# Kernel tuning notes

Hardware: AMD Instinct MI355X
Metric: run time of the kernel (lower is better)

## Reference

```python
import jax, jax.numpy as jnp
import numpy as np

EMBED = 1024
HEADS = 16
HEAD_DIM = EMBED // HEADS


def setup_inputs() -> dict:
    key = jax.random.key(0)
    k1, k2, k3 = jax.random.split(key, 3)
    return {
        "hidden_states": jax.random.normal(k1, (2, 2048, EMBED), dtype=jnp.float32),
        "c_attn_w": jax.random.normal(k2, (EMBED, 3 * EMBED), dtype=jnp.float32) * 0.02,
        "c_attn_b": jnp.zeros((3 * EMBED,), dtype=jnp.float32),
        "c_proj_w": jax.random.normal(k3, (EMBED, EMBED), dtype=jnp.float32) * 0.02,
        "c_proj_b": jnp.zeros((EMBED,), dtype=jnp.float32),
    }


def reference(hidden_states, c_attn_w, c_attn_b, c_proj_w, c_proj_b):
    B, S, E = hidden_states.shape
    H, D = HEADS, HEAD_DIM
    qkv = hidden_states @ c_attn_w + c_attn_b  # [B,S,3E]
    q, k, v = jnp.split(qkv, 3, axis=-1)
    # split heads -> [B,H,S,D]
    def split_heads(t):
        return t.reshape(B, S, H, D).transpose(0, 2, 1, 3)
    q, k, v = split_heads(q), split_heads(k), split_heads(v)
    scores = jnp.einsum("bhqd,bhkd->bhqk", q, k) / jnp.asarray(D ** 0.5, q.dtype)
    causal = jnp.tril(jnp.ones((S, S), dtype=bool))[None, None]
    mask_value = jnp.finfo(scores.dtype).min
    scores = jnp.where(causal, scores, mask_value)
    attn_weights = jax.nn.softmax(scores, axis=-1)  # [B,H,S,S]
    attn_out = jnp.einsum("bhqk,bhkd->bhqd", attn_weights, v)
    attn_out = attn_out.transpose(0, 2, 1, 3).reshape(B, S, E)
    attn_out = attn_out @ c_proj_w + c_proj_b
    return attn_out, attn_weights
```

## Files before the change

### kernel.cpp

```cpp
#include <hip/hip_runtime.h>
#include <hip/hip_bf16.h>

#define EMBED 1024
#define HEADS 16
#define HEAD_DIM 64
#define BATCH 2
#define SEQ 2048
#define MROWS (BATCH*SEQ)
#define NQKV  (3*EMBED)

typedef __attribute__((ext_vector_type(8))) short short8;
typedef __attribute__((ext_vector_type(4))) float float4v;

static __device__ __forceinline__ short f2bf(float f) {
    union { float f; unsigned u; } x; x.f = f;
    unsigned r = (x.u + 0x7FFFu + ((x.u >> 16) & 1u)) >> 16;
    return (short)r;
}

__global__ __launch_bounds__(256) void cast_bf16_k(const float* __restrict__ in,
                                                   short* __restrict__ out, int n8) {
    int i = blockIdx.x * 256 + threadIdx.x;
    if (i >= n8) return;
    const float4* p = (const float4*)in + (size_t)i * 2;
    float4 a = p[0], b = p[1];
    short8 o;
    o[0] = f2bf(a.x); o[1] = f2bf(a.y); o[2] = f2bf(a.z); o[3] = f2bf(a.w);
    o[4] = f2bf(b.x); o[5] = f2bf(b.y); o[6] = f2bf(b.z); o[7] = f2bf(b.w);
    *((short8*)out + i) = o;
}

__global__ __launch_bounds__(256) void transpose_cast_k(const float* __restrict__ W,
                                                        short* __restrict__ Wt,
                                                        int K, int N) {
    __shared__ float tile[32][33];
    int tx = threadIdx.x & 31, ty = threadIdx.x >> 5;
    int n0 = blockIdx.x * 32, k0 = blockIdx.y * 32;
#pragma unroll
    for (int i = 0; i < 4; i++)
        tile[ty + i * 8][tx] = W[(size_t)(k0 + ty + i * 8) * N + n0 + tx];
    __syncthreads();
#pragma unroll
    for (int i = 0; i < 4; i++)
        Wt[(size_t)(n0 + ty + i * 8) * K + k0 + tx] = f2bf(tile[tx][ty + i * 8]);
}

__global__ __launch_bounds__(256) void gemm_bf16_k(const short* __restrict__ A,
                                                   const short* __restrict__ Bt,
                                                   const float* __restrict__ bias,
                                                   float* __restrict__ outF,
                                                   short* __restrict__ outB,
                                                   int M, int N, int K) {
    __shared__ __align__(16) short As[64 * 40];
    __shared__ __align__(16) short Bs[64 * 40];
    const int tid = threadIdx.x;
    const int wave = tid >> 6, lane = tid & 63, quad = lane >> 4, l16 = lane & 15;
    const int m0 = blockIdx.x * 64, n0 = blockIdx.y * 64;

    float4v acc[4];
#pragma unroll
    for (int i = 0; i < 4; i++) acc[i] = (float4v){0.f, 0.f, 0.f, 0.f};

    const int r = tid >> 2, c8 = (tid & 3) * 8;
    for (int k0 = 0; k0 < K; k0 += 32) {
        __syncthreads();
        *(short8*)&As[r * 40 + c8] = *(const short8*)&A[(size_t)(m0 + r) * K + k0 + c8];
        *(short8*)&Bs[r * 40 + c8] = *(const short8*)&Bt[(size_t)(n0 + r) * K + k0 + c8];
        __syncthreads();
        short8 a = *(const short8*)&As[(wave * 16 + l16) * 40 + quad * 8];
#pragma unroll
        for (int ns = 0; ns < 4; ns++) {
            short8 b = *(const short8*)&Bs[(ns * 16 + l16) * 40 + quad * 8];
            acc[ns] = __builtin_amdgcn_mfma_f32_16x16x32_bf16(a, b, acc[ns], 0, 0, 0);
        }
    }
#pragma unroll
    for (int ns = 0; ns < 4; ns++) {
        int col = n0 + ns * 16 + l16;
        float bv = bias ? bias[col] : 0.f;
#pragma unroll
        for (int i = 0; i < 4; i++) {
            int row = m0 + wave * 16 + quad * 4 + i;
            float v = acc[ns][i] + bv;
            if (outF) outF[(size_t)row * N + col] = v;
            else      outB[(size_t)row * N + col] = f2bf(v);
        }
    }
}

__global__ __launch_bounds__(256) void attn_k(const short* __restrict__ qkv,
                                              float* __restrict__ wout,
                                              short* __restrict__ aheads) {
    __shared__ __align__(16) short Qs[32 * 72];
    __shared__ __align__(16) short Ks[32 * 72];
    __shared__ __align__(16) short Vt[64 * 40];
    __shared__ __align__(16) short Ps[32 * 40];
    __shared__ float Mred[2][32], Lred[2][32], Mfin[32], Lfin[32];

    const int tid = threadIdx.x;
    const int wave = tid >> 6, lane = tid & 63, quad = lane >> 4, l16 = lane & 15;
    const int qs = wave >> 1, ks = wave & 1;
    const int bh = blockIdx.x & 31;
    const int b = bh >> 4, h = bh & 15;
    const int qt = 63 - (blockIdx.x >> 5);
    const int q0 = qt * 32;
    const int kend = q0 + 32;
    const int nch = kend >> 5;

    const short* qbase = qkv + (size_t)(b * SEQ) * NQKV + h * 64;
    const short* kbase = qbase + EMBED;
    const short* vbase = qbase + 2 * EMBED;
    float* wrow = wout + ((size_t)bh * SEQ + q0) * SEQ;

    {
        int r = tid >> 3, c8 = (tid & 7) * 8;
        *(short8*)&Qs[r * 72 + c8] = *(const short8*)&qbase[(size_t)(q0 + r) * NQKV + c8];
    }
    __syncthreads();
    const short8 aq0 = *(const short8*)&Qs[(qs * 16 + l16) * 72 + quad * 8];
    const short8 aq1 = *(const short8*)&Qs[(qs * 16 + l16) * 72 + 32 + quad * 8];

    const int kcol = ks * 16 + l16;
    float mrun[4], lrun[4];
#pragma unroll
    for (int i = 0; i < 4; i++) { mrun[i] = -1e30f; lrun[i] = 0.f; }

    for (int c = 0; c < nch; c++) {
        int kc = c * 32;
        __syncthreads();
        {
            int r = tid >> 3, c8 = (tid & 7) * 8;
            *(short8*)&Ks[r * 72 + c8] = *(const short8*)&kbase[(size_t)(kc + r) * NQKV + c8];
        }
        __syncthreads();
        short8 bk0 = *(const short8*)&Ks[(ks * 16 + l16) * 72 + quad * 8];
        short8 bk1 = *(const short8*)&Ks[(ks * 16 + l16) * 72 + 32 + quad * 8];
        float4v acc = (float4v){0.f, 0.f, 0.f, 0.f};
        acc = __builtin_amdgcn_mfma_f32_16x16x32_bf16(aq0, bk0, acc, 0, 0, 0);
        acc = __builtin_amdgcn_mfma_f32_16x16x32_bf16(aq1, bk1, acc, 0, 0, 0);
        int kg = kc + kcol;
#pragma unroll
        for (int i = 0; i < 4; i++) {
            int qg = q0 + qs * 16 + quad * 4 + i;
            if (kg <= qg) {
                float s = acc[i] * 0.125f;
                float mn = fmaxf(mrun[i], s);
                lrun[i] = lrun[i] * __expf(mrun[i] - mn) + __expf(s - mn);
                mrun[i] = mn;
            }
        }
    }
#pragma unroll
    for (int i = 0; i < 4; i++) {
        float m = mrun[i], l = lrun[i];
#pragma unroll
        for (int off = 1; off <= 8; off <<= 1) {
            float mo = __shfl_xor(m, off);
            float lo = __shfl_xor(l, off);
            float mn = fmaxf(m, mo);
            l = l * __expf(m - mn) + lo * __expf(mo - mn);
            m = mn;
        }
        mrun[i] = m; lrun[i] = l;
    }
    if (l16 == 0) {
#pragma unroll
        for (int i = 0; i < 4; i++) {
            Mred[ks][qs * 16 + quad * 4 + i] = mrun[i];
            Lred[ks][qs * 16 + quad * 4 + i] = lrun[i];
        }
    }
    __syncthreads();
    if (tid < 32) {
        float m0 = Mred[0][tid], m1 = Mred[1][tid];
        float mn = fmaxf(m0, m1);
        float L = Lred[0][tid] * __expf(m0 - mn) + Lred[1][tid] * __expf(m1 - mn);
        Mfin[tid] = mn;
        Lfin[tid] = 1.0f / L;
    }
    __syncthreads();
    float Mi[4], Li[4];
#pragma unroll
    for (int i = 0; i < 4; i++) {
        Mi[i] = Mfin[qs * 16 + quad * 4 + i];
        Li[i] = Lfin[qs * 16 + quad * 4 + i];
    }

    float4v oacc0 = (float4v){0.f, 0.f, 0.f, 0.f};
    float4v oacc1 = (float4v){0.f, 0.f, 0.f, 0.f};
    const int dhalf = ks;
    for (int c = 0; c < nch; c++) {
        int kc = c * 32;
        __syncthreads();
        {
            int r = tid >> 3, c8 = (tid & 7) * 8;
            *(short8*)&Ks[r * 72 + c8] = *(const short8*)&kbase[(size_t)(kc + r) * NQKV + c8];
            int vk = tid & 31, dg = tid >> 5;
            short8 v8 = *(const short8*)&vbase[(size_t)(kc + vk) * NQKV + dg * 8];
#pragma unroll
            for (int i = 0; i < 8; i++) Vt[(dg * 8 + i) * 40 + vk] = v8[i];
        }
        __syncthreads();
        short8 bk0 = *(const short8*)&Ks[(ks * 16 + l16) * 72 + quad * 8];
        short8 bk1 = *(const short8*)&Ks[(ks * 16 + l16) * 72 + 32 + quad * 8];
        float4v acc = (float4v){0.f, 0.f, 0.f, 0.f};
        acc = __builtin_amdgcn_mfma_f32_16x16x32_bf16(aq0, bk0, acc, 0, 0, 0);
        acc = __builtin_amdgcn_mfma_f32_16x16x32_bf16(aq1, bk1, acc, 0, 0, 0);
        int kg = kc + kcol;
#pragma unroll
        for (int i = 0; i < 4; i++) {
            int lrow = qs * 16 + quad * 4 + i;
            int qg = q0 + lrow;
            float p = 0.f;
            if (kg <= qg) p = __expf(acc[i] * 0.125f - Mi[i]) * Li[i];
            wrow[(size_t)lrow * SEQ + kg] = p;
            Ps[lrow * 40 + ks * 16 + l16] = f2bf(p);
        }
        __syncthreads();
        short8 ap  = *(const short8*)&Ps[(qs * 16 + l16) * 40 + quad * 8];
        short8 bv0 = *(const short8*)&Vt[(dhalf * 32 + l16) * 40 + quad * 8];
        short8 bv1 = *(const short8*)&Vt[(dhalf * 32 + 16 + l16) * 40 + quad * 8];
        oacc0 = __builtin_amdgcn_mfma_f32_16x16x32_bf16(ap, bv0, oacc0, 0, 0, 0);
        oacc1 = __builtin_amdgcn_mfma_f32_16x16x32_bf16(ap, bv1, oacc1, 0, 0, 0);
    }

    int Z = SEQ - kend;
    if (Z > 0) {
        float4 z4 = make_float4(0.f, 0.f, 0.f, 0.f);
        for (int row = 0; row < 32; row++) {
            float* p = wrow + (size_t)row * SEQ + kend;
            for (int c4 = tid * 4; c4 < Z; c4 += 1024)
                *(float4*)(p + c4) = z4;
        }
    }

    short* obase = aheads + (size_t)(b * SEQ) * EMBED + h * 64;
#pragma unroll
    for (int i = 0; i < 4; i++) {
        int qg = q0 + qs * 16 + quad * 4 + i;
        obase[(size_t)qg * EMBED + dhalf * 32 + l16]      = f2bf(oacc0[i]);
        obase[(size_t)qg * EMBED + dhalf * 32 + 16 + l16] = f2bf(oacc1[i]);
    }
}

extern "C" void kernel_launch(void* const* d_in, const int* in_sizes, int n_in,
                              void* d_out, int out_size, void* d_ws, size_t ws_size,
                              hipStream_t stream) {
    const float* hidden = (const float*)d_in[0];
    const float* attn_w = (const float*)d_in[1];
    const float* attn_b = (const float*)d_in[2];
    const float* proj_w = (const float*)d_in[3];
    const float* proj_b = (const float*)d_in[4];

    float* out      = (float*)d_out;
    float* attn_out = out;
    float* weights  = out + (size_t)MROWS * EMBED;

    char* ws = (char*)d_ws;
    short* hid_b   = (short*)(ws);
    short* wqkv_t  = (short*)(ws + 8388608);
    short* wproj_t = (short*)(ws + 14680064);
    short* qkv     = (short*)(ws + 16777216);
    short* aheads  = (short*)(ws + 41943040);

    cast_bf16_k<<<dim3((MROWS * EMBED / 8 + 255) / 256), 256, 0, stream>>>(
        hidden, hid_b, MROWS * EMBED / 8);
    transpose_cast_k<<<dim3(NQKV / 32, EMBED / 32), 256, 0, stream>>>(
        attn_w, wqkv_t, EMBED, NQKV);
    transpose_cast_k<<<dim3(EMBED / 32, EMBED / 32), 256, 0, stream>>>(
        proj_w, wproj_t, EMBED, EMBED);
    gemm_bf16_k<<<dim3(MROWS / 64, NQKV / 64), 256, 0, stream>>>(
        hid_b, wqkv_t, attn_b, nullptr, qkv, MROWS, NQKV, EMBED);
    attn_k<<<dim3(BATCH * HEADS * (SEQ / 32)), 256, 0, stream>>>(
        qkv, weights, aheads);
    gemm_bf16_k<<<dim3(MROWS / 64, EMBED / 64), 256, 0, stream>>>(
        aheads, wproj_t, proj_b, attn_out, nullptr, MROWS, EMBED, EMBED);
}
```

Baseline: 777.3 us.

## Enlarge GEMM and attention tiles and use direct global-to-LDS loads

Replaces the 64x64 GEMM with a 128x128 tile kernel in which each wave computes a 64x64 sub-tile from 4x4 MFMAs. Operands are staged with global_load_lds, writing straight into LDS without passing through registers. The attention kernel moves from 32-row to 64-row query tiles with 64-key chunks. Each wave now owns 16 full query rows, which removes the cross-wave max/sum reduction through LDS and the syncs that went with it, and unmasked chunks skip the causal test. The aim is more MFMA work per byte loaded and fewer barriers, at the cost of more registers, fewer blocks, and the padding-free LDS layouts becoming prone to bank conflicts.

After: 725.1 us. 6.7% less time.

```diff
diff --git a/kernel.cpp b/kernel.cpp
--- a/kernel.cpp
+++ b/kernel.cpp
@@ -16,6 +16,12 @@
     union { float f; unsigned u; } x; x.f = f;
     unsigned r = (x.u + 0x7FFFu + ((x.u >> 16) & 1u)) >> 16;
     return (short)r;
+}
+
+static __device__ __forceinline__ void gl_lds16(const short* g, short* l) {
+    __builtin_amdgcn_global_load_lds(
+        (const __attribute__((address_space(1))) void*)g,
+        (__attribute__((address_space(3))) void*)l, 16, 0, 0);
 }
 
 __global__ __launch_bounds__(256) void cast_bf16_k(const float* __restrict__ in,
@@ -45,45 +51,70 @@
         Wt[(size_t)(n0 + ty + i * 8) * K + k0 + tx] = f2bf(tile[tx][ty + i * 8]);
 }
 
-__global__ __launch_bounds__(256) void gemm_bf16_k(const short* __restrict__ A,
-                                                   const short* __restrict__ Bt,
-                                                   const float* __restrict__ bias,
-                                                   float* __restrict__ outF,
-                                                   short* __restrict__ outB,
-                                                   int M, int N, int K) {
-    __shared__ __align__(16) short As[64 * 40];
-    __shared__ __align__(16) short Bs[64 * 40];
+__global__ __launch_bounds__(256) void gemm128_k(const short* __restrict__ A,
+                                                 const short* __restrict__ Bt,
+                                                 const float* __restrict__ bias,
+                                                 float* __restrict__ outF,
+                                                 short* __restrict__ outB,
+                                                 int M, int N, int K) {
+    __shared__ __align__(16) short As[128 * 32];
+    __shared__ __align__(16) short Bs[128 * 32];
     const int tid = threadIdx.x;
     const int wave = tid >> 6, lane = tid & 63, quad = lane >> 4, l16 = lane & 15;
-    const int m0 = blockIdx.x * 64, n0 = blockIdx.y * 64;
-
-    float4v acc[4];
-#pragma unroll
-    for (int i = 0; i < 4; i++) acc[i] = (float4v){0.f, 0.f, 0.f, 0.f};
-
-    const int r = tid >> 2, c8 = (tid & 3) * 8;
+    const int wm = wave >> 1, wn = wave & 1;
+    const int m0 = blockIdx.x * 128, n0 = blockIdx.y * 128;
+
+    float4v acc[4][4];
+#pragma unroll
+    for (int mi = 0; mi < 4; mi++)
+#pragma unroll
+        for (int ni = 0; ni < 4; ni++) acc[mi][ni] = (float4v){0.f, 0.f, 0.f, 0.f};
+
+    const int rA0 = wave * 32 + (lane >> 2), cA = (lane & 3) * 8;
+    const size_t arow0 = (size_t)(m0 + rA0) * K, arow1 = (size_t)(m0 + rA0 + 16) * K;
+    const size_t brow0 = (size_t)(n0 + rA0) * K, brow1 = (size_t)(n0 + rA0 + 16) * K;
+    short* ldsA0 = &As[(wave * 128 + lane) * 8];
+    short* ldsA1 = &As[(wave * 128 + 64 + lane) * 8];
+    short* ldsB0 = &Bs[(wave * 128 + lane) * 8];
+    short* ldsB1 = &Bs[(wave * 128 + 64 + lane) * 8];
+
     for (int k0 = 0; k0 < K; k0 += 32) {
         __syncthreads();
-        *(short8*)&As[r * 40 + c8] = *(const short8*)&A[(size_t)(m0 + r) * K + k0 + c8];
-        *(short8*)&Bs[r * 40 + c8] = *(const short8*)&Bt[(size_t)(n0 + r) * K + k0 + c8];
-        __syncthreads();
-        short8 a = *(const short8*)&As[(wave * 16 + l16) * 40 + quad * 8];
-#pragma unroll
-        for (int ns = 0; ns < 4; ns++) {
-            short8 b = *(const short8*)&Bs[(ns * 16 + l16) * 40 + quad * 8];
-            acc[ns] = __builtin_amdgcn_mfma_f32_16x16x32_bf16(a, b, acc[ns], 0, 0, 0);
-        }
-    }
-#pragma unroll
-    for (int ns = 0; ns < 4; ns++) {
-        int col = n0 + ns * 16 + l16;
+        gl_lds16(A + arow0 + k0 + cA, ldsA0);
+        gl_lds16(A + arow1 + k0 + cA, ldsA1);
+        gl_lds16(Bt + brow0 + k0 + cA, ldsB0);
+        gl_lds16(Bt + brow1 + k0 + cA, ldsB1);
+        __syncthreads();
+        short8 a[4], b[4];
+#pragma unroll
+        for (int mi = 0; mi < 4; mi++)
+            a[mi] = *(const short8*)&As[(wm * 64 + mi * 16 + l16) * 32 + quad * 8];
+#pragma unroll
+        for (int ni = 0; ni < 4; ni++)
+            b[ni] = *(const short8*)&Bs[(wn * 64 + ni * 16 + l16) * 32 + quad * 8];
+#pragma unroll
+        for (int mi = 0; mi < 4; mi++)
+#pragma unroll
+            for (int ni = 0; ni < 4; ni++)
+                acc[mi][ni] = __builtin_amdgcn_mfma_f32_16x16x32_bf16(a[mi], b[ni], acc[mi][ni], 0, 0, 0);
+    }
+
+#pragma unroll
+    for (int ni = 0; ni < 4; ni++) {
+        int col = n0 + wn * 64 + ni * 16 + l16;
         float bv = bias ? bias[col] : 0.f;
 #pragma unroll
-        for (int i = 0; i < 4; i++) {
-            int row = m0 + wave * 16 + quad * 4 + i;
-            float v = acc[ns][i] + bv;
-            if (outF) outF[(size_t)row * N + col] = v;
-            else      outB[(size_t)row * N + col] = f2bf(v);
+        for (int mi = 0; mi < 4; mi++) {
+            int row = m0 + wm * 64 + mi * 16 + quad * 4;
+            if (outF) {
+#pragma unroll
+                for (int i = 0; i < 4; i++)
+                    outF[(size_t)(row + i) * N + col] = acc[mi][ni][i] + bv;
+            } else {
+#pragma unroll
+                for (int i = 0; i < 4; i++)
+                    outB[(size_t)(row + i) * N + col] = f2bf(acc[mi][ni][i] + bv);
+            }
         }
     }
 }
@@ -91,21 +122,18 @@
 __global__ __launch_bounds__(256) void attn_k(const short* __restrict__ qkv,
                                               float* __restrict__ wout,
                                               short* __restrict__ aheads) {
-    __shared__ __align__(16) short Qs[32 * 72];
-    __shared__ __align__(16) short Ks[32 * 72];
-    __shared__ __align__(16) short Vt[64 * 40];
-    __shared__ __align__(16) short Ps[32 * 40];
-    __shared__ float Mred[2][32], Lred[2][32], Mfin[32], Lfin[32];
+    __shared__ __align__(16) short Qs[2][64 * 32];
+    __shared__ __align__(16) short Ks[2][64 * 32];
+    __shared__ __align__(16) short Vt[64 * 72];
+    __shared__ __align__(16) short Ps[64 * 72];
 
     const int tid = threadIdx.x;
     const int wave = tid >> 6, lane = tid & 63, quad = lane >> 4, l16 = lane & 15;
-    const int qs = wave >> 1, ks = wave & 1;
     const int bh = blockIdx.x & 31;
     const int b = bh >> 4, h = bh & 15;
-    const int qt = 63 - (blockIdx.x >> 5);
-    const int q0 = qt * 32;
-    const int kend = q0 + 32;
-    const int nch = kend >> 5;
+    const int qt = 31 - (blockIdx.x >> 5);
+    const int q0 = qt * 64;
+    const int nch = qt + 1;
 
     const short* qbase = qkv + (size_t)(b * SEQ) * NQKV + h * 64;
     const short* kbase = qbase + EMBED;
@@ -113,133 +141,158 @@
     float* wrow = wout + ((size_t)bh * SEQ + q0) * SEQ;
 
     {
-        int r = tid >> 3, c8 = (tid & 7) * 8;
-        *(short8*)&Qs[r * 72 + c8] = *(const short8*)&qbase[(size_t)(q0 + r) * NQKV + c8];
+        const int r = lane >> 2, c = (lane & 3) * 8;
+        gl_lds16(qbase + (size_t)(q0 + wave * 16 + r) * NQKV + c,
+                 &Qs[0][(wave * 64 + lane) * 8]);
+        gl_lds16(qbase + (size_t)(q0 + wave * 16 + r) * NQKV + 32 + c,
+                 &Qs[1][(wave * 64 + lane) * 8]);
     }
     __syncthreads();
-    const short8 aq0 = *(const short8*)&Qs[(qs * 16 + l16) * 72 + quad * 8];
-    const short8 aq1 = *(const short8*)&Qs[(qs * 16 + l16) * 72 + 32 + quad * 8];
-
-    const int kcol = ks * 16 + l16;
-    float mrun[4], lrun[4];
-#pragma unroll
-    for (int i = 0; i < 4; i++) { mrun[i] = -1e30f; lrun[i] = 0.f; }
+    short8 aq0 = *(const short8*)&Qs[0][(wave * 16 + l16) * 32 + quad * 8];
+    short8 aq1 = *(const short8*)&Qs[1][(wave * 16 + l16) * 32 + quad * 8];
+
+    const int kr = lane >> 2, kc16 = (lane & 3) * 8;
+    const int vkp = (tid & 31) * 2, vd8 = (tid >> 5) * 8;
+
+    float m[4], l[4];
+#pragma unroll
+    for (int i = 0; i < 4; i++) { m[i] = -1e30f; l[i] = 0.f; }
 
     for (int c = 0; c < nch; c++) {
-        int kc = c * 32;
-        __syncthreads();
+        const int kc = c * 64;
+        __syncthreads();
+        gl_lds16(kbase + (size_t)(kc + wave * 16 + kr) * NQKV + kc16,
+                 &Ks[0][(wave * 64 + lane) * 8]);
+        gl_lds16(kbase + (size_t)(kc + wave * 16 + kr) * NQKV + 32 + kc16,
+                 &Ks[1][(wave * 64 + lane) * 8]);
+        __syncthreads();
+        float4v sc[4];
+#pragma unroll
+        for (int kg = 0; kg < 4; kg++) {
+            short8 bk0 = *(const short8*)&Ks[0][(kg * 16 + l16) * 32 + quad * 8];
+            short8 bk1 = *(const short8*)&Ks[1][(kg * 16 + l16) * 32 + quad * 8];
+            float4v s = (float4v){0.f, 0.f, 0.f, 0.f};
+            s = __builtin_amdgcn_mfma_f32_16x16x32_bf16(aq0, bk0, s, 0, 0, 0);
+            s = __builtin_amdgcn_mfma_f32_16x16x32_bf16(aq1, bk1, s, 0, 0, 0);
+            sc[kg] = s;
+        }
+        if (c < qt) {
+#pragma unroll
+            for (int i = 0; i < 4; i++) {
+                float mx = m[i];
+#pragma unroll
+                for (int kg = 0; kg < 4; kg++) mx = fmaxf(mx, sc[kg][i] * 0.125f);
+                float s0 = 0.f;
+#pragma unroll
+                for (int kg = 0; kg < 4; kg++) s0 += __expf(sc[kg][i] * 0.125f - mx);
+                l[i] = l[i] * __expf(m[i] - mx) + s0;
+                m[i] = mx;
+            }
+        } else {
+#pragma unroll
+            for (int i = 0; i < 4; i++) {
+                int qrl = wave * 16 + quad * 4 + i;
+                float mx = m[i];
+#pragma unroll
+                for (int kg = 0; kg < 4; kg++)
+                    if (kg * 16 + l16 <= qrl) mx = fmaxf(mx, sc[kg][i] * 0.125f);
+                float s0 = 0.f;
+#pragma unroll
+                for (int kg = 0; kg < 4; kg++)
+                    if (kg * 16 + l16 <= qrl) s0 += __expf(sc[kg][i] * 0.125f - mx);
+                l[i] = l[i] * __expf(m[i] - mx) + s0;
+                m[i] = mx;
+            }
+        }
+    }
+    float Mi[4], Li[4];
+#pragma unroll
+    for (int i = 0; i < 4; i++) {
+        float mm = m[i], ll = l[i];
+#pragma unroll
+        for (int off = 1; off <= 8; off <<= 1) {
+            float mo = __shfl_xor(mm, off);
+            float lo = __shfl_xor(ll, off);
+            float mn = fmaxf(mm, mo);
+            ll = ll * __expf(mm - mn) + lo * __expf(mo - mn);
+            mm = mn;
+        }
+        Mi[i] = mm; Li[i] = 1.0f / ll;
+    }
+
+    float4v oacc[4];
+#pragma unroll
+    for (int dg = 0; dg < 4; dg++) oacc[dg] = (float4v){0.f, 0.f, 0.f, 0.f};
+
+    for (int c = 0; c < nch; c++) {
+        const int kc = c * 64;
+        __syncthreads();
+        gl_lds16(kbase + (size_t)(kc + wave * 16 + kr) * NQKV + kc16,
+                 &Ks[0][(wave * 64 + lane) * 8]);
+        gl_lds16(kbase + (size_t)(kc + wave * 16 + kr) * NQKV + 32 + kc16,
+                 &Ks[1][(wave * 64 + lane) * 8]);
         {
-            int r = tid >> 3, c8 = (tid & 7) * 8;
-            *(short8*)&Ks[r * 72 + c8] = *(const short8*)&kbase[(size_t)(kc + r) * NQKV + c8];
-        }
-        __syncthreads();
-        short8 bk0 = *(const short8*)&Ks[(ks * 16 + l16) * 72 + quad * 8];
-        short8 bk1 = *(const short8*)&Ks[(ks * 16 + l16) * 72 + 32 + quad * 8];
-        float4v acc = (float4v){0.f, 0.f, 0.f, 0.f};
-        acc = __builtin_amdgcn_mfma_f32_16x16x32_bf16(aq0, bk0, acc, 0, 0, 0);
-        acc = __builtin_amdgcn_mfma_f32_16x16x32_bf16(aq1, bk1, acc, 0, 0, 0);
-        int kg = kc + kcol;
+            short8 va = *(const short8*)&vbase[(size_t)(kc + vkp) * NQKV + vd8];
+            short8 vb = *(const short8*)&vbase[(size_t)(kc + vkp + 1) * NQKV + vd8];
+#pragma unroll
+            for (int i = 0; i < 8; i++) {
+                short2 pk; pk.x = va[i]; pk.y = vb[i];
+                *(short2*)&Vt[(vd8 + i) * 72 + vkp] = pk;
+            }
+        }
+        __syncthreads();
+        float4v sc[4];
+#pragma unroll
+        for (int kg = 0; kg < 4; kg++) {
+            short8 bk0 = *(const short8*)&Ks[0][(kg * 16 + l16) * 32 + quad * 8];
+            short8 bk1 = *(const short8*)&Ks[1][(kg * 16 + l16) * 32 + quad * 8];
+            float4v s = (float4v){0.f, 0.f, 0.f, 0.f};
+            s = __builtin_amdgcn_mfma_f32_16x16x32_bf16(aq0, bk0, s, 0, 0, 0);
+            s = __builtin_amdgcn_mfma_f32_16x16x32_bf16(aq1, bk1, s, 0, 0, 0);
+            sc[kg] = s;
+        }
+        const bool diag = (c == qt);
 #pragma unroll
         for (int i = 0; i < 4; i++) {
-            int qg = q0 + qs * 16 + quad * 4 + i;
-            if (kg <= qg) {
-                float s = acc[i] * 0.125f;
-                float mn = fmaxf(mrun[i], s);
-                lrun[i] = lrun[i] * __expf(mrun[i] - mn) + __expf(s - mn);
-                mrun[i] = mn;
-            }
-        }
-    }
+            int lrow = wave * 16 + quad * 4 + i;
+            float* wr = wrow + (size_t)lrow * SEQ + kc;
+#pragma unroll
+            for (int kg = 0; kg < 4; kg++) {
+                float p = 0.f;
+                if (!diag || (kg * 16 + l16 <= lrow))
+                    p = __expf(sc[kg][i] * 0.125f - Mi[i]) * Li[i];
+                wr[kg * 16 + l16] = p;
+                Ps[lrow * 72 + kg * 16 + l16] = f2bf(p);
+            }
+        }
+#pragma unroll
+        for (int kh = 0; kh < 2; kh++) {
+            short8 ap = *(const short8*)&Ps[(wave * 16 + l16) * 72 + kh * 32 + quad * 8];
+#pragma unroll
+            for (int dg = 0; dg < 4; dg++) {
+                short8 bv = *(const short8*)&Vt[(dg * 16 + l16) * 72 + kh * 32 + quad * 8];
+                oacc[dg] = __builtin_amdgcn_mfma_f32_16x16x32_bf16(ap, bv, oacc[dg], 0, 0, 0);
+            }
+        }
+    }
+
+    const int kend = (qt + 1) * 64;
+    if (kend < SEQ) {
+        float4 z4 = make_float4(0.f, 0.f, 0.f, 0.f);
+        for (int row = 0; row < 64; row++) {
+            float* p = wrow + (size_t)row * SEQ;
+            for (int cc = kend + tid * 4; cc < SEQ; cc += 1024)
+                *(float4*)(p + cc) = z4;
+        }
+    }
+
+    short* obase = aheads + (size_t)(b * SEQ) * EMBED + h * 64;
 #pragma unroll
     for (int i = 0; i < 4; i++) {
-        float m = mrun[i], l = lrun[i];
-#pragma unroll
-        for (int off = 1; off <= 8; off <<= 1) {
-            float mo = __shfl_xor(m, off);
-            float lo = __shfl_xor(l, off);
-            float mn = fmaxf(m, mo);
-            l = l * __expf(m - mn) + lo * __expf(mo - mn);
-            m = mn;
-        }
-        mrun[i] = m; lrun[i] = l;
-    }
-    if (l16 == 0) {
-#pragma unroll
-        for (int i = 0; i < 4; i++) {
-            Mred[ks][qs * 16 + quad * 4 + i] = mrun[i];
-            Lred[ks][qs * 16 + quad * 4 + i] = lrun[i];
-        }
-    }
-    __syncthreads();
-    if (tid < 32) {
-        float m0 = Mred[0][tid], m1 = Mred[1][tid];
-        float mn = fmaxf(m0, m1);
-        float L = Lred[0][tid] * __expf(m0 - mn) + Lred[1][tid] * __expf(m1 - mn);
-        Mfin[tid] = mn;
-        Lfin[tid] = 1.0f / L;
-    }
-    __syncthreads();
-    float Mi[4], Li[4];
-#pragma unroll
-    for (int i = 0; i < 4; i++) {
-        Mi[i] = Mfin[qs * 16 + quad * 4 + i];
-        Li[i] = Lfin[qs * 16 + quad * 4 + i];
-    }
-
-    float4v oacc0 = (float4v){0.f, 0.f, 0.f, 0.f};
-    float4v oacc1 = (float4v){0.f, 0.f, 0.f, 0.f};
-    const int dhalf = ks;
-    for (int c = 0; c < nch; c++) {
-        int kc = c * 32;
-        __syncthreads();
-        {
-            int r = tid >> 3, c8 = (tid & 7) * 8;
-            *(short8*)&Ks[r * 72 + c8] = *(const short8*)&kbase[(size_t)(kc + r) * NQKV + c8];
-            int vk = tid & 31, dg = tid >> 5;
-            short8 v8 = *(const short8*)&vbase[(size_t)(kc + vk) * NQKV + dg * 8];
-#pragma unroll
-            for (int i = 0; i < 8; i++) Vt[(dg * 8 + i) * 40 + vk] = v8[i];
-        }
-        __syncthreads();
-        short8 bk0 = *(const short8*)&Ks[(ks * 16 + l16) * 72 + quad * 8];
-        short8 bk1 = *(const short8*)&Ks[(ks * 16 + l16) * 72 + 32 + quad * 8];
-        float4v acc = (float4v){0.f, 0.f, 0.f, 0.f};
-        acc = __builtin_amdgcn_mfma_f32_16x16x32_bf16(aq0, bk0, acc, 0, 0, 0);
-        acc = __builtin_amdgcn_mfma_f32_16x16x32_bf16(aq1, bk1, acc, 0, 0, 0);
-        int kg = kc + kcol;
-#pragma unroll
-        for (int i = 0; i < 4; i++) {
-            int lrow = qs * 16 + quad * 4 + i;
-            int qg = q0 + lrow;
-            float p = 0.f;
-            if (kg <= qg) p = __expf(acc[i] * 0.125f - Mi[i]) * Li[i];
-            wrow[(size_t)lrow * SEQ + kg] = p;
-            Ps[lrow * 40 + ks * 16 + l16] = f2bf(p);
-        }
-        __syncthreads();
-        short8 ap  = *(const short8*)&Ps[(qs * 16 + l16) * 40 + quad * 8];
-        short8 bv0 = *(const short8*)&Vt[(dhalf * 32 + l16) * 40 + quad * 8];
-        short8 bv1 = *(const short8*)&Vt[(dhalf * 32 + 16 + l16) * 40 + quad * 8];
-        oacc0 = __builtin_amdgcn_mfma_f32_16x16x32_bf16(ap, bv0, oacc0, 0, 0, 0);
-        oacc1 = __builtin_amdgcn_mfma_f32_16x16x32_bf16(ap, bv1, oacc1, 0, 0, 0);
-    }
-
-    int Z = SEQ - kend;
-    if (Z > 0) {
-        float4 z4 = make_float4(0.f, 0.f, 0.f, 0.f);
-        for (int row = 0; row < 32; row++) {
-            float* p = wrow + (size_t)row * SEQ + kend;
-            for (int c4 = tid * 4; c4 < Z; c4 += 1024)
-                *(float4*)(p + c4) = z4;
-        }
-    }
-
-    short* obase = aheads + (size_t)(b * SEQ) * EMBED + h * 64;
-#pragma unroll
-    for (int i = 0; i < 4; i++) {
-        int qg = q0 + qs * 16 + quad * 4 + i;
-        obase[(size_t)qg * EMBED + dhalf * 32 + l16]      = f2bf(oacc0[i]);
-        obase[(size_t)qg * EMBED + dhalf * 32 + 16 + l16] = f2bf(oacc1[i]);
+        int qg = q0 + wave * 16 + quad * 4 + i;
+#pragma unroll
+        for (int dg = 0; dg < 4; dg++)
+            obase[(size_t)qg * EMBED + dg * 16 + l16] = f2bf(oacc[dg][i]);
     }
 }
 
@@ -269,10 +322,10 @@
         attn_w, wqkv_t, EMBED, NQKV);
     transpose_cast_k<<<dim3(EMBED / 32, EMBED / 32), 256, 0, stream>>>(
         proj_w, wproj_t, EMBED, EMBED);
-    gemm_bf16_k<<<dim3(MROWS / 64, NQKV / 64), 256, 0, stream>>>(
+    gemm128_k<<<dim3(MROWS / 128, NQKV / 128), 256, 0, stream>>>(
         hid_b, wqkv_t, attn_b, nullptr, qkv, MROWS, NQKV, EMBED);
-    attn_k<<<dim3(BATCH * HEADS * (SEQ / 32)), 256, 0, stream>>>(
+    attn_k<<<dim3(BATCH * HEADS * (SEQ / 64)), 256, 0, stream>>>(
         qkv, weights, aheads);
-    gemm_bf16_k<<<dim3(MROWS / 64, EMBED / 64), 256, 0, stream>>>(
+    gemm128_k<<<dim3(MROWS / 128, EMBED / 128), 256, 0, stream>>>(
         aheads, wproj_t, proj_b, attn_out, nullptr, MROWS, EMBED, EMBED);
 }
```
